# Kernel tuning notes

Hardware: AMD Instinct MI355X
Metric: run time of the kernel (lower is better)

## Reference

```python
import jax, jax.numpy as jnp
import numpy as np

B, N, D_IN, D_OUT, H, ALPHA = 8, 2048, 128, 64, 1, 0.2


def setup_inputs() -> dict:
    key = jax.random.key(0)
    k1, k2, k3, k4 = jax.random.split(key, 4)
    x = jax.random.normal(k1, (B, N, D_IN), dtype=jnp.float32)
    adj = jax.random.randint(k2, (B, N, N), 0, 2, dtype=jnp.int32)
    # guarantee self-loops so no softmax row is entirely masked
    adj = jnp.maximum(adj, jnp.eye(N, dtype=jnp.int32)[None])
    # xavier_uniform with gain=1.414, as in the torch module
    lim_w = 1.414 * np.sqrt(6.0 / (D_IN + D_OUT * H))
    W = jax.random.uniform(k3, (D_OUT * H, D_IN), minval=-lim_w, maxval=lim_w, dtype=jnp.float32)
    b = jnp.zeros((D_OUT * H,), dtype=jnp.float32)
    lim_a = 1.414 * np.sqrt(6.0 / (H + 2 * D_OUT))
    a = jax.random.uniform(k4, (H, 2 * D_OUT), minval=-lim_a, maxval=lim_a, dtype=jnp.float32)
    return {"x": x, "adj_hat": adj, "W": W, "b": b, "a": a}


def reference(x, adj_hat, W, b, a):
    Bn, Nn = x.shape[:2]
    # projection: [B,N,d_in] -> [B,N,H,D]
    xp = (x @ W.T + b).reshape(Bn, Nn, H, D_OUT)
    # additive score a . [x_i ; x_j] split into two O(N) dot-products
    # (mathematically identical to the original O(N^2) concat formulation)
    a_src, a_dst = a[:, :D_OUT], a[:, D_OUT:]
    e_src = jnp.einsum('bnhd,hd->bnh', xp, a_src)  # score contribution of node i (query/p axis)
    e_dst = jnp.einsum('bnhd,hd->bnh', xp, a_dst)  # score contribution of node j (neighbor/q axis)
    e = e_src[:, :, None, :] + e_dst[:, None, :, :]  # [B,N,N,H]
    e = jax.nn.leaky_relu(e, ALPHA)
    e = jnp.where(adj_hat[..., None] == 0, -jnp.inf, e)
    att = jax.nn.softmax(e, axis=2)  # softmax over neighbor axis (torch dim=-2)
    res = jnp.einsum('bmnh,bnhd->bmhd', att, xp)  # weighted aggregation
    return res.reshape(Bn, Nn, H * D_OUT)  # concat_heads=True
```

## Files before the change

### kernel.cpp

```cpp
#include <hip/hip_runtime.h>
#include <hip/hip_bf16.h>
#include <cstdint>

#define NN 2048
#define BB 8
#define DIN 128
#define DOUT 64
#define PHN 256
#define NPH (NN / PHN)
#define PCH 130

typedef __attribute__((ext_vector_type(8))) short bf16x8;
typedef __attribute__((ext_vector_type(4))) float f32x4;

static __device__ __forceinline__ unsigned short f2b(float f) {
    union { __hip_bfloat16 h; unsigned short s; } u;
    u.h = __float2bfloat16(f);
    return u.s;
}

__global__ __launch_bounds__(256) void gat_xp_mfma(
    const float* __restrict__ x, const float* __restrict__ W,
    const float* __restrict__ bias, const float* __restrict__ a,
    unsigned short* __restrict__ xpT, float* __restrict__ e_src,
    float* __restrict__ e_dst)
{
    __shared__ float red[4 * 16 * 65];
    const int t = threadIdx.x;
    const int lane = t & 63;
    const int w = t >> 6;
    const int lr = lane & 15;
    const int g  = lane >> 4;
    const int r0 = blockIdx.x * 16;
    const int k0 = w * 32 + g * 8;

    const float* xr = x + (size_t)(r0 + lr) * DIN + k0;
    const float4 xa = *(const float4*)xr;
    const float4 xb4 = *(const float4*)(xr + 4);
    bf16x8 afr;
    afr[0]=f2b(xa.x);  afr[1]=f2b(xa.y);  afr[2]=f2b(xa.z);  afr[3]=f2b(xa.w);
    afr[4]=f2b(xb4.x); afr[5]=f2b(xb4.y); afr[6]=f2b(xb4.z); afr[7]=f2b(xb4.w);

    #pragma unroll
    for (int dt = 0; dt < 4; ++dt) {
        const float* wr = W + (size_t)(dt * 16 + lr) * DIN + k0;
        const float4 wa = *(const float4*)wr;
        const float4 wb = *(const float4*)(wr + 4);
        bf16x8 bfr;
        bfr[0]=f2b(wa.x); bfr[1]=f2b(wa.y); bfr[2]=f2b(wa.z); bfr[3]=f2b(wa.w);
        bfr[4]=f2b(wb.x); bfr[5]=f2b(wb.y); bfr[6]=f2b(wb.z); bfr[7]=f2b(wb.w);
        f32x4 acc = {0.f, 0.f, 0.f, 0.f};
        acc = __builtin_amdgcn_mfma_f32_16x16x32_bf16(afr, bfr, acc, 0, 0, 0);
        #pragma unroll
        for (int reg = 0; reg < 4; ++reg)
            red[w * 1040 + (g * 4 + reg) * 65 + dt * 16 + lr] = acc[reg];
    }
    __syncthreads();

    const int row = t >> 4;
    const int dq  = t & 15;
    const int b   = r0 >> 11;
    const int nb  = r0 & (NN - 1);
    float es = 0.f, ed = 0.f;
    #pragma unroll
    for (int j = 0; j < 4; ++j) {
        const int d = dq * 4 + j;
        const float v = red[0 * 1040 + row * 65 + d] + red[1 * 1040 + row * 65 + d]
                      + red[2 * 1040 + row * 65 + d] + red[3 * 1040 + row * 65 + d]
                      + bias[d];
        es += v * a[d];
        ed += v * a[DOUT + d];
        xpT[((size_t)(b * DOUT + d) << 11) + nb + row] = f2b(v);
    }
    es += __shfl_xor(es, 1); es += __shfl_xor(es, 2);
    es += __shfl_xor(es, 4); es += __shfl_xor(es, 8);
    ed += __shfl_xor(ed, 1); ed += __shfl_xor(ed, 2);
    ed += __shfl_xor(ed, 4); ed += __shfl_xor(ed, 8);
    if (dq == 0) {
        e_src[r0 + row] = es;
        e_dst[r0 + row] = ed;
    }
}

__global__ __launch_bounds__(256) void gat_attn_mfma(
    const int* __restrict__ adj, const unsigned short* __restrict__ xpT,
    const float* __restrict__ e_src, const float* __restrict__ e_dst,
    float* __restrict__ out)
{
    __shared__ float d_lds[NN];
    __shared__ unsigned short p_lds[2][32 * PCH];
    __shared__ float mred[4];
    __shared__ float s_lds[16];
    __shared__ float bnd_lds[16];
    __shared__ float rs_lds[16];

    const int t = threadIdx.x;
    const int lane = t & 63;
    const int w = t >> 6;
    const int lr = lane & 15;
    const int g  = lane >> 4;
    const int b  = blockIdx.x >> 7;
    const int m0 = (blockIdx.x & 127) * 16;
    const size_t base = (size_t)b * NN;

    float dm = -1e30f;
    #pragma unroll
    for (int i = 0; i < 8; ++i) {
        const float v = e_dst[base + i * 256 + t];
        d_lds[i * 256 + t] = v;
        dm = fmaxf(dm, v);
    }
    #pragma unroll
    for (int off = 32; off >= 1; off >>= 1) dm = fmaxf(dm, __shfl_xor(dm, off));
    if (lane == 0) mred[w] = dm;
    __syncthreads();
    const float dmax = fmaxf(fmaxf(mred[0], mred[1]), fmaxf(mred[2], mred[3]));
    if (t < 16) {
        const float s = e_src[base + m0 + t];
        const float e0 = s + dmax;
        s_lds[t] = s;
        bnd_lds[t] = fmaxf(e0, 0.2f * e0);
    }
    __syncthreads();

    float srow[4], brow[4];
    const int* aptr[4];
    #pragma unroll
    for (int it = 0; it < 4; ++it) {
        const int row = it * 4 + w;
        srow[it] = s_lds[row];
        brow[it] = bnd_lds[row];
        aptr[it] = adj + ((base + (size_t)(m0 + row)) << 11) + lane * 4;
    }

    int4 acur[4], anxt[4];
    #pragma unroll
    for (int it = 0; it < 4; ++it) acur[it] = *(const int4*)(aptr[it]);

    f32x4 acc = {0.f, 0.f, 0.f, 0.f};
    float rs_acc[4] = {0.f, 0.f, 0.f, 0.f};
    const unsigned short* xb = xpT + ((size_t)(b * DOUT + w * 16 + lr) << 11);

    const int c  = lane >> 1;
    const int jj = (lane & 1) * 4;

    int buf = 0;
    for (int ph = 0; ph < NPH; ++ph) {
        if (ph + 1 < NPH) {
            #pragma unroll
            for (int it = 0; it < 4; ++it)
                anxt[it] = *(const int4*)(aptr[it] + (ph + 1) * PHN);
        }
        const float4 dv = *(const float4*)(d_lds + ph * PHN + lane * 4);
        const float dvv[4] = {dv.x, dv.y, dv.z, dv.w};
        unsigned short* pb = &p_lds[buf][0];
        #pragma unroll
        for (int it = 0; it < 4; ++it) {
            const int row = it * 4 + w;
            const float s = srow[it], bd = brow[it];
            const int av[4] = {acur[it].x, acur[it].y, acur[it].z, acur[it].w};
            float p[4];
            #pragma unroll
            for (int j = 0; j < 4; ++j) {
                const float e = s + dvv[j];
                const float le = fmaxf(e, 0.2f * e);
                const float pe = __expf(le - bd);
                p[j] = av[j] ? pe : 0.f;
            }
            rs_acc[it] += p[0] + p[1] + p[2] + p[3];
            unsigned int* pp32 =
                (unsigned int*)(pb + c * PCH + row * 8 + jj);
            pp32[0] = ((unsigned)f2b(p[1]) << 16) | f2b(p[0]);
            pp32[1] = ((unsigned)f2b(p[3]) << 16) | f2b(p[2]);
        }
        __syncthreads();
        const unsigned int* pw = (const unsigned int*)pb;
        const int nb0 = ph * PHN;
        #pragma unroll
        for (int ks = 0; ks < 8; ++ks) {
            const int cc = ks * 4 + g;
            const int wbase = cc * 65 + lr * 4;
            union { unsigned int u[4]; bf16x8 v; } af;
            af.u[0] = pw[wbase + 0];
            af.u[1] = pw[wbase + 1];
            af.u[2] = pw[wbase + 2];
            af.u[3] = pw[wbase + 3];
            const bf16x8 bfr = *(const bf16x8*)(xb + nb0 + ks * 32 + g * 8);
            acc = __builtin_amdgcn_mfma_f32_16x16x32_bf16(af.v, bfr, acc, 0, 0, 0);
        }
        #pragma unroll
        for (int it = 0; it < 4; ++it) acur[it] = anxt[it];
        buf ^= 1;
    }

    #pragma unroll
    for (int it = 0; it < 4; ++it) {
        float v = rs_acc[it];
        #pragma unroll
        for (int off = 32; off >= 1; off >>= 1) v += __shfl_xor(v, off);
        if (lane == 0) rs_lds[it * 4 + w] = v;
    }
    __syncthreads();

    #pragma unroll
    for (int reg = 0; reg < 4; ++reg) {
        const int row = g * 4 + reg;
        const float o = acc[reg] / rs_lds[row];
        out[(base + (size_t)(m0 + row)) * DOUT + w * 16 + lr] = o;
    }
}

extern "C" void kernel_launch(void* const* d_in, const int* in_sizes, int n_in,
                              void* d_out, int out_size, void* d_ws, size_t ws_size,
                              hipStream_t stream) {
    const float* x    = (const float*)d_in[0];
    const int*   adj  = (const int*)d_in[1];
    const float* W    = (const float*)d_in[2];
    const float* bvec = (const float*)d_in[3];
    const float* a    = (const float*)d_in[4];
    float* out = (float*)d_out;

    unsigned short* xpT = (unsigned short*)d_ws;
    float* e_src = (float*)((char*)d_ws + (1 << 21));
    float* e_dst = e_src + (size_t)BB * NN;

    gat_xp_mfma<<<(BB * NN) / 16, 256, 0, stream>>>(x, W, bvec, a, xpT, e_src, e_dst);
    gat_attn_mfma<<<BB * (NN / 16), 256, 0, stream>>>(adj, xpT, e_src, e_dst, out);
}
```

Measured before the change: 214.7 us.

## Deepen adjacency prefetch to two phases and hoist xpT fragment loads

The adjacency loads move ahead of the e_dst max reduction and are now issued two phases ahead through a three-register ring instead of one phase ahead. All eight xpT B-fragments for a phase are loaded at the start of the phase, so their latency overlaps the exp and softmax work. The __syncthreads is replaced by an explicit lgkmcnt wait plus s_barrier, the MFMA block is raised to priority 1, and launch bounds ask for 4 blocks per CU. The aim is to hide HBM latency on the int32 adjacency stream, at the cost of more registers, which the occupancy hint may turn into spills.

```diff
diff --git a/kernel.cpp b/kernel.cpp
--- a/kernel.cpp
+++ b/kernel.cpp
@@ -82,7 +82,7 @@
     }
 }
 
-__global__ __launch_bounds__(256) void gat_attn_mfma(
+__global__ __launch_bounds__(256, 4) void gat_attn_mfma(
     const int* __restrict__ adj, const unsigned short* __restrict__ xpT,
     const float* __restrict__ e_src, const float* __restrict__ e_dst,
     float* __restrict__ out)
@@ -103,6 +103,17 @@
     const int m0 = (blockIdx.x & 127) * 16;
     const size_t base = (size_t)b * NN;
 
+    const int* aptr[4];
+    #pragma unroll
+    for (int it = 0; it < 4; ++it)
+        aptr[it] = adj + ((base + (size_t)(m0 + it * 4 + w)) << 11) + lane * 4;
+
+    int4 acur[4], amid[4], anew[4];
+    #pragma unroll
+    for (int it = 0; it < 4; ++it) acur[it] = *(const int4*)(aptr[it]);
+    #pragma unroll
+    for (int it = 0; it < 4; ++it) amid[it] = *(const int4*)(aptr[it] + PHN);
+
     float dm = -1e30f;
     #pragma unroll
     for (int i = 0; i < 8; ++i) {
@@ -124,18 +135,11 @@
     __syncthreads();
 
     float srow[4], brow[4];
-    const int* aptr[4];
     #pragma unroll
     for (int it = 0; it < 4; ++it) {
-        const int row = it * 4 + w;
-        srow[it] = s_lds[row];
-        brow[it] = bnd_lds[row];
-        aptr[it] = adj + ((base + (size_t)(m0 + row)) << 11) + lane * 4;
-    }
-
-    int4 acur[4], anxt[4];
-    #pragma unroll
-    for (int it = 0; it < 4; ++it) acur[it] = *(const int4*)(aptr[it]);
+        srow[it] = s_lds[it * 4 + w];
+        brow[it] = bnd_lds[it * 4 + w];
+    }
 
     f32x4 acc = {0.f, 0.f, 0.f, 0.f};
     float rs_acc[4] = {0.f, 0.f, 0.f, 0.f};
@@ -144,16 +148,23 @@
     const int c  = lane >> 1;
     const int jj = (lane & 1) * 4;
 
-    int buf = 0;
     for (int ph = 0; ph < NPH; ++ph) {
-        if (ph + 1 < NPH) {
+        const int nb0 = ph * PHN;
+
+        bf16x8 bfr[8];
+        #pragma unroll
+        for (int ks = 0; ks < 8; ++ks)
+            bfr[ks] = *(const bf16x8*)(xb + nb0 + ks * 32 + g * 8);
+
+        if (ph + 2 < NPH) {
             #pragma unroll
             for (int it = 0; it < 4; ++it)
-                anxt[it] = *(const int4*)(aptr[it] + (ph + 1) * PHN);
+                anew[it] = *(const int4*)(aptr[it] + (ph + 2) * PHN);
         }
-        const float4 dv = *(const float4*)(d_lds + ph * PHN + lane * 4);
+
+        const float4 dv = *(const float4*)(d_lds + nb0 + lane * 4);
         const float dvv[4] = {dv.x, dv.y, dv.z, dv.w};
-        unsigned short* pb = &p_lds[buf][0];
+        unsigned short* pb = &p_lds[ph & 1][0];
         #pragma unroll
         for (int it = 0; it < 4; ++it) {
             const int row = it * 4 + w;
@@ -167,30 +178,31 @@
                 const float pe = __expf(le - bd);
                 p[j] = av[j] ? pe : 0.f;
             }
-            rs_acc[it] += p[0] + p[1] + p[2] + p[3];
-            unsigned int* pp32 =
-                (unsigned int*)(pb + c * PCH + row * 8 + jj);
+            rs_acc[it] += (p[0] + p[1]) + (p[2] + p[3]);
+            unsigned int* pp32 = (unsigned int*)(pb + c * PCH + row * 8 + jj);
             pp32[0] = ((unsigned)f2b(p[1]) << 16) | f2b(p[0]);
             pp32[1] = ((unsigned)f2b(p[3]) << 16) | f2b(p[2]);
         }
-        __syncthreads();
+
+        asm volatile("s_waitcnt lgkmcnt(0)" ::: "memory");
+        __builtin_amdgcn_s_barrier();
+
         const unsigned int* pw = (const unsigned int*)pb;
-        const int nb0 = ph * PHN;
+        __builtin_amdgcn_s_setprio(1);
         #pragma unroll
         for (int ks = 0; ks < 8; ++ks) {
-            const int cc = ks * 4 + g;
-            const int wbase = cc * 65 + lr * 4;
+            const int wbase = (ks * 4 + g) * 65 + lr * 4;
             union { unsigned int u[4]; bf16x8 v; } af;
             af.u[0] = pw[wbase + 0];
             af.u[1] = pw[wbase + 1];
             af.u[2] = pw[wbase + 2];
             af.u[3] = pw[wbase + 3];
-            const bf16x8 bfr = *(const bf16x8*)(xb + nb0 + ks * 32 + g * 8);
-            acc = __builtin_amdgcn_mfma_f32_16x16x32_bf16(af.v, bfr, acc, 0, 0, 0);
+            acc = __builtin_amdgcn_mfma_f32_16x16x32_bf16(af.v, bfr[ks], acc, 0, 0, 0);
         }
-        #pragma unroll
-        for (int it = 0; it < 4; ++it) acur[it] = anxt[it];
-        buf ^= 1;
+        __builtin_amdgcn_s_setprio(0);
+
+        #pragma unroll
+        for (int it = 0; it < 4; ++it) { acur[it] = amid[it]; amid[it] = anew[it]; }
     }
 
     #pragma unroll
```

After: 227.3 us. 5.9% more time.

## Bitpack adjacency mask in LDS and store xp in MFMA fragment layout

Applied to the files above, without the earlier changes.

The attention kernel now streams each block's 16 adjacency rows once, packs them into a 32-bit mask per 32 columns in LDS, and has each wave compute its own bf16 probabilities directly in registers as MFMA A-fragments, dropping the shared P buffer and per-phase barriers. The projection kernel processes 32 rows per block and writes xp in a fragment-major layout so each lane issues one contiguous 16-byte load per k-step. The cost is that every wave recomputes exp for all 16 rows (four times the redundant exp work), and the adjacency load now happens before any compute starts.

```diff
diff --git a/kernel.cpp b/kernel.cpp
--- a/kernel.cpp
+++ b/kernel.cpp
@@ -6,9 +6,6 @@
 #define BB 8
 #define DIN 128
 #define DOUT 64
-#define PHN 256
-#define NPH (NN / PHN)
-#define PCH 130
 
 typedef __attribute__((ext_vector_type(8))) short bf16x8;
 typedef __attribute__((ext_vector_type(4))) float f32x4;
@@ -22,77 +19,100 @@
 __global__ __launch_bounds__(256) void gat_xp_mfma(
     const float* __restrict__ x, const float* __restrict__ W,
     const float* __restrict__ bias, const float* __restrict__ a,
-    unsigned short* __restrict__ xpT, float* __restrict__ e_src,
+    unsigned short* __restrict__ xpF, float* __restrict__ e_src,
     float* __restrict__ e_dst)
 {
-    __shared__ float red[4 * 16 * 65];
+    __shared__ float red[4 * 32 * 65];
     const int t = threadIdx.x;
     const int lane = t & 63;
     const int w = t >> 6;
     const int lr = lane & 15;
     const int g  = lane >> 4;
-    const int r0 = blockIdx.x * 16;
+    const int r0 = blockIdx.x * 32;
     const int k0 = w * 32 + g * 8;
 
-    const float* xr = x + (size_t)(r0 + lr) * DIN + k0;
-    const float4 xa = *(const float4*)xr;
-    const float4 xb4 = *(const float4*)(xr + 4);
-    bf16x8 afr;
-    afr[0]=f2b(xa.x);  afr[1]=f2b(xa.y);  afr[2]=f2b(xa.z);  afr[3]=f2b(xa.w);
-    afr[4]=f2b(xb4.x); afr[5]=f2b(xb4.y); afr[6]=f2b(xb4.z); afr[7]=f2b(xb4.w);
-
+    bf16x8 bfr[4];
     #pragma unroll
     for (int dt = 0; dt < 4; ++dt) {
         const float* wr = W + (size_t)(dt * 16 + lr) * DIN + k0;
         const float4 wa = *(const float4*)wr;
         const float4 wb = *(const float4*)(wr + 4);
-        bf16x8 bfr;
-        bfr[0]=f2b(wa.x); bfr[1]=f2b(wa.y); bfr[2]=f2b(wa.z); bfr[3]=f2b(wa.w);
-        bfr[4]=f2b(wb.x); bfr[5]=f2b(wb.y); bfr[6]=f2b(wb.z); bfr[7]=f2b(wb.w);
-        f32x4 acc = {0.f, 0.f, 0.f, 0.f};
-        acc = __builtin_amdgcn_mfma_f32_16x16x32_bf16(afr, bfr, acc, 0, 0, 0);
-        #pragma unroll
-        for (int reg = 0; reg < 4; ++reg)
-            red[w * 1040 + (g * 4 + reg) * 65 + dt * 16 + lr] = acc[reg];
+        bfr[dt][0]=f2b(wa.x); bfr[dt][1]=f2b(wa.y); bfr[dt][2]=f2b(wa.z); bfr[dt][3]=f2b(wa.w);
+        bfr[dt][4]=f2b(wb.x); bfr[dt][5]=f2b(wb.y); bfr[dt][6]=f2b(wb.z); bfr[dt][7]=f2b(wb.w);
+    }
+    #pragma unroll
+    for (int half = 0; half < 2; ++half) {
+        const float* xr = x + (size_t)(r0 + half * 16 + lr) * DIN + k0;
+        const float4 xa = *(const float4*)xr;
+        const float4 xb4 = *(const float4*)(xr + 4);
+        bf16x8 afr;
+        afr[0]=f2b(xa.x);  afr[1]=f2b(xa.y);  afr[2]=f2b(xa.z);  afr[3]=f2b(xa.w);
+        afr[4]=f2b(xb4.x); afr[5]=f2b(xb4.y); afr[6]=f2b(xb4.z); afr[7]=f2b(xb4.w);
+        #pragma unroll
+        for (int dt = 0; dt < 4; ++dt) {
+            f32x4 acc = {0.f, 0.f, 0.f, 0.f};
+            acc = __builtin_amdgcn_mfma_f32_16x16x32_bf16(afr, bfr[dt], acc, 0, 0, 0);
+            #pragma unroll
+            for (int reg = 0; reg < 4; ++reg)
+                red[w * 2080 + (half * 16 + g * 4 + reg) * 65 + dt * 16 + lr] = acc[reg];
+        }
     }
     __syncthreads();
 
-    const int row = t >> 4;
-    const int dq  = t & 15;
-    const int b   = r0 >> 11;
-    const int nb  = r0 & (NN - 1);
-    float es = 0.f, ed = 0.f;
-    #pragma unroll
-    for (int j = 0; j < 4; ++j) {
-        const int d = dq * 4 + j;
-        const float v = red[0 * 1040 + row * 65 + d] + red[1 * 1040 + row * 65 + d]
-                      + red[2 * 1040 + row * 65 + d] + red[3 * 1040 + row * 65 + d]
-                      + bias[d];
-        es += v * a[d];
-        ed += v * a[DOUT + d];
-        xpT[((size_t)(b * DOUT + d) << 11) + nb + row] = f2b(v);
-    }
-    es += __shfl_xor(es, 1); es += __shfl_xor(es, 2);
-    es += __shfl_xor(es, 4); es += __shfl_xor(es, 8);
-    ed += __shfl_xor(ed, 1); ed += __shfl_xor(ed, 2);
-    ed += __shfl_xor(ed, 4); ed += __shfl_xor(ed, 8);
-    if (dq == 0) {
-        e_src[r0 + row] = es;
-        e_dst[r0 + row] = ed;
+    const int b  = r0 >> 11;
+    const int kb = (r0 & (NN - 1)) >> 5;
+
+    #pragma unroll
+    for (int i = 0; i < 2; ++i) {
+        const int row = i * 16 + (t >> 4);
+        const int dq  = t & 15;
+        float es = 0.f, ed = 0.f;
+        #pragma unroll
+        for (int j = 0; j < 4; ++j) {
+            const int d = dq * 4 + j;
+            const float v = red[0 * 2080 + row * 65 + d] + red[1 * 2080 + row * 65 + d]
+                          + red[2 * 2080 + row * 65 + d] + red[3 * 2080 + row * 65 + d]
+                          + bias[d];
+            es += v * a[d];
+            ed += v * a[DOUT + d];
+        }
+        es += __shfl_xor(es, 1); es += __shfl_xor(es, 2);
+        es += __shfl_xor(es, 4); es += __shfl_xor(es, 8);
+        ed += __shfl_xor(ed, 1); ed += __shfl_xor(ed, 2);
+        ed += __shfl_xor(ed, 4); ed += __shfl_xor(ed, 8);
+        if (dq == 0) {
+            e_src[r0 + row] = es;
+            e_dst[r0 + row] = ed;
+        }
+    }
+
+    {
+        const int dt = w;
+        const int d  = dt * 16 + lr;
+        const float bv = bias[d];
+        bf16x8 frag;
+        #pragma unroll
+        for (int j = 0; j < 8; ++j) {
+            const int row = g * 8 + j;
+            const float v = red[0 * 2080 + row * 65 + d] + red[1 * 2080 + row * 65 + d]
+                          + red[2 * 2080 + row * 65 + d] + red[3 * 2080 + row * 65 + d]
+                          + bv;
+            frag[j] = f2b(v);
+        }
+        *(bf16x8*)(xpF + ((size_t)((b * 4 + dt) * 64 + kb) << 9) + lane * 8) = frag;
     }
 }
 
 __global__ __launch_bounds__(256) void gat_attn_mfma(
-    const int* __restrict__ adj, const unsigned short* __restrict__ xpT,
+    const int* __restrict__ adj, const unsigned short* __restrict__ xpF,
     const float* __restrict__ e_src, const float* __restrict__ e_dst,
     float* __restrict__ out)
 {
     __shared__ float d_lds[NN];
-    __shared__ unsigned short p_lds[2][32 * PCH];
+    __shared__ unsigned int mk[16 * 65];
     __shared__ float mred[4];
     __shared__ float s_lds[16];
     __shared__ float bnd_lds[16];
-    __shared__ float rs_lds[16];
 
     const int t = threadIdx.x;
     const int lane = t & 63;
@@ -102,6 +122,21 @@
     const int b  = blockIdx.x >> 7;
     const int m0 = (blockIdx.x & 127) * 16;
     const size_t base = (size_t)b * NN;
+
+    const int* __restrict__ arow = adj + ((base + m0) << 11);
+    #pragma unroll 4
+    for (int s = 0; s < 32; ++s) {
+        const int f = s * 1024 + t * 4;
+        const int4 v = *(const int4*)(arow + f);
+        unsigned int wv = ((v.x != 0) ? 1u : 0u) | ((v.y != 0) ? 2u : 0u)
+                        | ((v.z != 0) ? 4u : 0u) | ((v.w != 0) ? 8u : 0u);
+        wv <<= ((t & 7) * 4);
+        wv |= __shfl_xor(wv, 1);
+        wv |= __shfl_xor(wv, 2);
+        wv |= __shfl_xor(wv, 4);
+        if ((t & 7) == 0)
+            mk[(f >> 11) * 65 + ((f & (NN - 1)) >> 5)] = wv;
+    }
 
     float dm = -1e30f;
     #pragma unroll
@@ -123,90 +158,42 @@
     }
     __syncthreads();
 
-    float srow[4], brow[4];
-    const int* aptr[4];
-    #pragma unroll
-    for (int it = 0; it < 4; ++it) {
-        const int row = it * 4 + w;
-        srow[it] = s_lds[row];
-        brow[it] = bnd_lds[row];
-        aptr[it] = adj + ((base + (size_t)(m0 + row)) << 11) + lane * 4;
-    }
-
-    int4 acur[4], anxt[4];
-    #pragma unroll
-    for (int it = 0; it < 4; ++it) acur[it] = *(const int4*)(aptr[it]);
+    const float sreg = s_lds[lr];
+    const float bnd  = bnd_lds[lr];
 
     f32x4 acc = {0.f, 0.f, 0.f, 0.f};
-    float rs_acc[4] = {0.f, 0.f, 0.f, 0.f};
-    const unsigned short* xb = xpT + ((size_t)(b * DOUT + w * 16 + lr) << 11);
-
-    const int c  = lane >> 1;
-    const int jj = (lane & 1) * 4;
-
-    int buf = 0;
-    for (int ph = 0; ph < NPH; ++ph) {
-        if (ph + 1 < NPH) {
-            #pragma unroll
-            for (int it = 0; it < 4; ++it)
-                anxt[it] = *(const int4*)(aptr[it] + (ph + 1) * PHN);
-        }
-        const float4 dv = *(const float4*)(d_lds + ph * PHN + lane * 4);
-        const float dvv[4] = {dv.x, dv.y, dv.z, dv.w};
-        unsigned short* pb = &p_lds[buf][0];
-        #pragma unroll
-        for (int it = 0; it < 4; ++it) {
-            const int row = it * 4 + w;
-            const float s = srow[it], bd = brow[it];
-            const int av[4] = {acur[it].x, acur[it].y, acur[it].z, acur[it].w};
-            float p[4];
-            #pragma unroll
-            for (int j = 0; j < 4; ++j) {
-                const float e = s + dvv[j];
-                const float le = fmaxf(e, 0.2f * e);
-                const float pe = __expf(le - bd);
-                p[j] = av[j] ? pe : 0.f;
-            }
-            rs_acc[it] += p[0] + p[1] + p[2] + p[3];
-            unsigned int* pp32 =
-                (unsigned int*)(pb + c * PCH + row * 8 + jj);
-            pp32[0] = ((unsigned)f2b(p[1]) << 16) | f2b(p[0]);
-            pp32[1] = ((unsigned)f2b(p[3]) << 16) | f2b(p[2]);
-        }
-        __syncthreads();
-        const unsigned int* pw = (const unsigned int*)pb;
-        const int nb0 = ph * PHN;
-        #pragma unroll
-        for (int ks = 0; ks < 8; ++ks) {
-            const int cc = ks * 4 + g;
-            const int wbase = cc * 65 + lr * 4;
-            union { unsigned int u[4]; bf16x8 v; } af;
-            af.u[0] = pw[wbase + 0];
-            af.u[1] = pw[wbase + 1];
-            af.u[2] = pw[wbase + 2];
-            af.u[3] = pw[wbase + 3];
-            const bf16x8 bfr = *(const bf16x8*)(xb + nb0 + ks * 32 + g * 8);
-            acc = __builtin_amdgcn_mfma_f32_16x16x32_bf16(af.v, bfr, acc, 0, 0, 0);
-        }
-        #pragma unroll
-        for (int it = 0; it < 4; ++it) acur[it] = anxt[it];
-        buf ^= 1;
-    }
-
-    #pragma unroll
-    for (int it = 0; it < 4; ++it) {
-        float v = rs_acc[it];
-        #pragma unroll
-        for (int off = 32; off >= 1; off >>= 1) v += __shfl_xor(v, off);
-        if (lane == 0) rs_lds[it * 4 + w] = v;
-    }
-    __syncthreads();
+    float rs = 0.f;
+    const unsigned short* __restrict__ xv =
+        xpF + ((size_t)((b * 4 + w) * 64) << 9) + lane * 8;
+
+    #pragma unroll 8
+    for (int ks = 0; ks < 64; ++ks) {
+        const unsigned int mw = mk[lr * 65 + ks];
+        const float4 d0 = *(const float4*)(d_lds + ks * 32 + g * 8);
+        const float4 d1 = *(const float4*)(d_lds + ks * 32 + g * 8 + 4);
+        const float dvv[8] = {d0.x, d0.y, d0.z, d0.w, d1.x, d1.y, d1.z, d1.w};
+        bf16x8 afr;
+        #pragma unroll
+        for (int j = 0; j < 8; ++j) {
+            const float e = sreg + dvv[j];
+            const float le = fmaxf(e, 0.2f * e);
+            const float pe = __expf(le - bnd);
+            const float p = ((mw >> (g * 8 + j)) & 1u) ? pe : 0.f;
+            rs += p;
+            afr[j] = f2b(p);
+        }
+        const bf16x8 bfr = *(const bf16x8*)(xv + (size_t)ks * 512);
+        acc = __builtin_amdgcn_mfma_f32_16x16x32_bf16(afr, bfr, acc, 0, 0, 0);
+    }
+
+    rs += __shfl_xor(rs, 16);
+    rs += __shfl_xor(rs, 32);
 
     #pragma unroll
     for (int reg = 0; reg < 4; ++reg) {
         const int row = g * 4 + reg;
-        const float o = acc[reg] / rs_lds[row];
-        out[(base + (size_t)(m0 + row)) * DOUT + w * 16 + lr] = o;
+        const float nrm = __shfl(rs, row);
+        out[(base + (size_t)(m0 + row)) * DOUT + w * 16 + lr] = acc[reg] / nrm;
     }
 }
 
@@ -220,10 +207,10 @@
     const float* a    = (const float*)d_in[4];
     float* out = (float*)d_out;
 
-    unsigned short* xpT = (unsigned short*)d_ws;
+    unsigned short* xpF = (unsigned short*)d_ws;
     float* e_src = (float*)((char*)d_ws + (1 << 21));
     float* e_dst = e_src + (size_t)BB * NN;
 
-    gat_xp_mfma<<<(BB * NN) / 16, 256, 0, stream>>>(x, W, bvec, a, xpT, e_src, e_dst);
-    gat_attn_mfma<<<BB * (NN / 16), 256, 0, stream>>>(adj, xpT, e_src, e_dst, out);
-}
+    gat_xp_mfma<<<(BB * NN) / 32, 256, 0, stream>>>(x, W, bvec, a, xpF, e_src, e_dst);
+    gat_attn_mfma<<<BB * (NN / 16), 256, 0, stream>>>(adj, xpF, e_src, e_dst, out);
+}
```

Result: slower. 253.8 us (+18.2%).
